# Optimization experiments

Hardware: AMD Instinct MI355X
Metric: run time of the kernel (lower is better)

Reference implementation:

```python
import jax, jax.numpy as jnp
import numpy as np

B, C, D = 2, 2048, 1024   # batch, seq_len, hidden_size
I = 2048                  # intermediate_size (GLU hidden)
E, K = 8, 2               # n_experts, top_k
CF = 1.25                 # capacity factor


def setup_inputs() -> dict:
    key = jax.random.key(0)
    k1, k2, k3, k4 = jax.random.split(key, 4)
    scale = 0.02
    return {
        "hidden_states": jax.random.normal(k1, (B, C, D), jnp.float32),
        "Wg": jax.random.normal(k2, (E, D), jnp.float32) * scale,      # router gate weight [E, d]
        "W1": jax.random.normal(k3, (E, D, 2 * I), jnp.float32) * scale,  # expert in-proj
        "W2": jax.random.normal(k4, (E, I, D), jnp.float32) * scale,      # expert out-proj
    }


def reference(hidden_states, Wg, W1, W2):
    Bx, Cx, d = hidden_states.shape
    N = Bx * Cx
    cap = int(N * K * CF / E)  # exp_capacity (static)
    x = hidden_states.reshape(N, d)

    # --- router (eval mode: no noise) ---
    logits = x @ Wg.T                          # [N, E]
    top_v, top_i = jax.lax.top_k(logits, K)    # [N, K]
    gates = jax.nn.softmax(top_v, axis=-1)     # [N, K]

    # --- greedy capacity-limited assignment (token-major, then k), vectorized ---
    flat_e = top_i.reshape(N * K)              # expert id per (token, k) slot, in loop order
    gates_f = gates.reshape(N * K)
    tok = jnp.repeat(jnp.arange(N), K)         # token id per slot
    onehot = jax.nn.one_hot(flat_e, E, dtype=jnp.int32)
    pos = jnp.cumsum(onehot, axis=0) - 1       # running count per expert
    pos_f = jnp.take_along_axis(pos, flat_e[:, None], axis=1)[:, 0]
    keep = pos_f < cap                         # slots beyond capacity are dropped
    pos_safe = jnp.where(keep, pos_f, cap)     # out-of-range -> dropped by mode='drop'

    # --- dispatch: exp_batches[e, pos] = x[token] ---
    exp_batches = jnp.zeros((E, cap, d), x.dtype).at[flat_e, pos_safe].set(x[tok], mode='drop')

    # --- per-expert GLU MLP (batched over experts) ---
    h = jnp.einsum('ecd,edf->ecf', exp_batches, W1)       # [E, cap, 2I]
    inp, gate = jnp.split(h, 2, axis=-1)
    h = jax.nn.gelu(inp, approximate=False) * gate        # exact gelu, matches torch
    exp_out = jnp.einsum('eci,eid->ecd', h, W2)           # [E, cap, d]

    # --- combine: equals exp_mask.view(N,-1) @ exp_out.view(-1,d) ---
    gathered = exp_out[flat_e, jnp.minimum(pos_safe, cap - 1)]  # [N*K, d]
    contrib = jnp.where(keep, gates_f, 0.0)[:, None] * gathered
    out = jax.ops.segment_sum(contrib, tok, num_segments=N)    # [N, d]
    return out.reshape(Bx, Cx, d)
```

## Files before the change

### kernel.cpp

```cpp
#include <hip/hip_runtime.h>
#include <hip/hip_bf16.h>
#include <math.h>

#define N_TOK 4096
#define DIM   1024
#define NEXP  8
#define IDIM  2048
#define TWOI  4096
#define CAP   1280

#define W1_BLOCKS (64 * 16 * NEXP)
#define W2_BLOCKS (16 * 32 * NEXP)

using short8  = __attribute__((ext_vector_type(8))) short;
using floatx4 = __attribute__((ext_vector_type(4))) float;

__device__ __forceinline__ unsigned short f2b(float f) {
  __hip_bfloat16 h = __float2bfloat16(f);
  return *reinterpret_cast<unsigned short*>(&h);
}

__device__ __forceinline__ void async16(const unsigned short* g, unsigned short* l) {
  __builtin_amdgcn_global_load_lds(
      (const __attribute__((address_space(1))) unsigned int*)g,
      (__attribute__((address_space(3))) unsigned int*)l,
      16, 0, 0);
}

__global__ __launch_bounds__(256) void trans_kernel(const float* __restrict__ W1,
                                                    const float* __restrict__ W2,
                                                    unsigned short* __restrict__ w1t,
                                                    unsigned short* __restrict__ w2t) {
  __shared__ float tile[64][65];
  int bid = blockIdx.x;
  const float* s; unsigned short* d; int R, C, r0, c0;
  if (bid < W1_BLOCKS) {
    int e = bid >> 10;
    int t = bid & 1023;
    R = DIM; C = TWOI;
    r0 = (t & 15) * 64;
    c0 = (t >> 4) * 64;
    s = W1 + (size_t)e * R * C;
    d = w1t + (size_t)e * R * C;
  } else {
    int b2 = bid - W1_BLOCKS;
    int e = b2 >> 9;
    int t = b2 & 511;
    R = IDIM; C = DIM;
    r0 = (t & 31) * 64;
    c0 = (t >> 5) * 64;
    s = W2 + (size_t)e * R * C;
    d = w2t + (size_t)e * R * C;
  }
  int tid = threadIdx.x;
  int tr = tid >> 4, tc = (tid & 15) * 4;
#pragma unroll
  for (int i = 0; i < 4; i++) {
    float4 v = *reinterpret_cast<const float4*>(&s[(size_t)(r0 + tr + i * 16) * C + c0 + tc]);
    tile[tr + i * 16][tc]     = v.x;
    tile[tr + i * 16][tc + 1] = v.y;
    tile[tr + i * 16][tc + 2] = v.z;
    tile[tr + i * 16][tc + 3] = v.w;
  }
  __syncthreads();
#pragma unroll
  for (int j = 0; j < 4; j++) {
    int c = (tid >> 4) + j * 16;
    int r4 = (tid & 15) * 4;
    ushort4 o;
    o.x = f2b(tile[r4][c]);
    o.y = f2b(tile[r4 + 1][c]);
    o.z = f2b(tile[r4 + 2][c]);
    o.w = f2b(tile[r4 + 3][c]);
    *reinterpret_cast<ushort4*>(&d[(size_t)(c0 + c) * R + r0 + r4]) = o;
  }
}

__global__ __launch_bounds__(256) void router_kernel(const float* __restrict__ x,
                                                     const float* __restrict__ Wg,
                                                     unsigned short* __restrict__ xb,
                                                     float* __restrict__ out,
                                                     int* __restrict__ top_i,
                                                     float* __restrict__ gates) {
  __shared__ float wg[NEXP * DIM];
  int tid = threadIdx.x;
  for (int i = tid * 4; i < NEXP * DIM; i += 256 * 4) {
    *reinterpret_cast<float4*>(wg + i) = *reinterpret_cast<const float4*>(Wg + i);
  }
  __syncthreads();
  int wave = tid >> 6, lane = tid & 63;
  int t = blockIdx.x * 4 + wave;
  const float* xr = x + (size_t)t * DIM;
  unsigned short* xbr = xb + (size_t)t * DIM;
  float* outr = out + (size_t)t * DIM;
  double acc[NEXP];
#pragma unroll
  for (int e = 0; e < NEXP; e++) acc[e] = 0.0;
  for (int i = lane; i < DIM; i += 64) {
    float xf = xr[i];
    xbr[i] = f2b(xf);
    outr[i] = 0.0f;
    double xv = (double)xf;
#pragma unroll
    for (int e = 0; e < NEXP; e++) acc[e] += xv * (double)wg[e * DIM + i];
  }
#pragma unroll
  for (int e = 0; e < NEXP; e++) {
#pragma unroll
    for (int m = 1; m < 64; m <<= 1) acc[e] += __shfl_xor(acc[e], m, 64);
  }
  if (lane == 0) {
    int i0 = 0; double v0 = acc[0];
    for (int e = 1; e < NEXP; e++) { if (acc[e] > v0) { v0 = acc[e]; i0 = e; } }
    int i1 = -1; double v1 = -1e300;
    for (int e = 0; e < NEXP; e++) { if (e != i0 && acc[e] > v1) { v1 = acc[e]; i1 = e; } }
    double e1 = exp(v1 - v0);
    float g0 = (float)(1.0 / (1.0 + e1));
    float g1 = (float)(e1 / (1.0 + e1));
    top_i[t * 2] = i0; top_i[t * 2 + 1] = i1;
    gates[t * 2] = g0; gates[t * 2 + 1] = g1;
  }
}

__global__ __launch_bounds__(1024) void scan_kernel(const int* __restrict__ top_i,
                                                    const float* __restrict__ gates,
                                                    int* __restrict__ rowtok,
                                                    float* __restrict__ rowgate,
                                                    int* __restrict__ cnt) {
  __shared__ int hist[NEXP][1024];
  int t = threadIdx.x;
  int s0 = t * 8;
  int eloc[8];
  int c[NEXP];
#pragma unroll
  for (int e = 0; e < NEXP; e++) c[e] = 0;
#pragma unroll
  for (int j = 0; j < 8; j++) { int e = top_i[s0 + j]; eloc[j] = e; c[e]++; }
#pragma unroll
  for (int e = 0; e < NEXP; e++) hist[e][t] = c[e];
  __syncthreads();
  for (int step = 1; step < 1024; step <<= 1) {
    int tmp[NEXP];
#pragma unroll
    for (int e = 0; e < NEXP; e++) tmp[e] = (t >= step) ? hist[e][t - step] : 0;
    __syncthreads();
#pragma unroll
    for (int e = 0; e < NEXP; e++) hist[e][t] += tmp[e];
    __syncthreads();
  }
  int base[NEXP];
#pragma unroll
  for (int e = 0; e < NEXP; e++) base[e] = hist[e][t] - c[e];
  if (t < NEXP) {
    int tot = hist[t][1023];
    cnt[t] = tot < CAP ? tot : CAP;
  }
#pragma unroll
  for (int j = 0; j < 8; j++) {
    int s = s0 + j;
    int e = eloc[j];
    int pos = base[e]++;
    if (pos < CAP) {
      rowtok[e * CAP + pos] = s >> 1;
      rowgate[e * CAP + pos] = gates[s];
    }
  }
}

__global__ __launch_bounds__(256, 3) void gemm1_kernel(const unsigned short* __restrict__ xb,
                                                       const unsigned short* __restrict__ w1t,
                                                       const int* __restrict__ rowtok,
                                                       const int* __restrict__ cnt,
                                                       unsigned short* __restrict__ H) {
  int e  = blockIdx.z;
  int m0 = blockIdx.y * 128;
  int i0 = blockIdx.x * 64;
  int cnte = cnt[e];
  if (m0 >= cnte) return;

  __shared__ __align__(16) unsigned short As[128 * 32];
  __shared__ __align__(16) unsigned short Bi[64 * 32];
  __shared__ __align__(16) unsigned short Bg[64 * 32];

  int tid  = threadIdx.x;
  int lane = tid & 63;
  int wave = tid >> 6;

  int srA0 = wave * 32 + (lane >> 2);
  int srA1 = srA0 + 16;
  int srB  = wave * 16 + (lane >> 2);
  int sk   = (lane & 3) * 8;

  int ma0 = m0 + srA0, ma1 = m0 + srA1;
  int tok0 = (ma0 < cnte) ? rowtok[e * CAP + ma0] : 0;
  int tok1 = (ma1 < cnte) ? rowtok[e * CAP + ma1] : 0;

  const unsigned short* w1e = w1t + (size_t)e * TWOI * DIM;
  const unsigned short* gA0 = xb + (size_t)tok0 * DIM + sk;
  const unsigned short* gA1 = xb + (size_t)tok1 * DIM + sk;
  const unsigned short* gBi = w1e + (size_t)(i0 + srB) * DIM + sk;
  const unsigned short* gBg = w1e + (size_t)(i0 + srB + IDIM) * DIM + sk;

  unsigned short* lA0 = As + (wave * 2 + 0) * 512;
  unsigned short* lA1 = As + (wave * 2 + 1) * 512;
  unsigned short* lBi = Bi + wave * 512;
  unsigned short* lBg = Bg + wave * 512;

  int lane16 = lane & 15;
  int quad   = lane >> 4;
  int wm = (wave & 1) * 64;
  int wn = (wave >> 1) * 32;

  floatx4 acc_i[4][2], acc_g[4][2];
#pragma unroll
  for (int i = 0; i < 4; i++)
#pragma unroll
    for (int j = 0; j < 2; j++) {
      acc_i[i][j] = (floatx4){0.f, 0.f, 0.f, 0.f};
      acc_g[i][j] = (floatx4){0.f, 0.f, 0.f, 0.f};
    }

  for (int k0 = 0; k0 < DIM; k0 += 32) {
    __syncthreads();
    async16(gA0 + k0, lA0);
    async16(gA1 + k0, lA1);
    async16(gBi + k0, lBi);
    async16(gBg + k0, lBg);
    __syncthreads();

    short8 a[4];
#pragma unroll
    for (int i = 0; i < 4; i++)
      a[i] = *(const short8*)&As[(wm + i * 16 + lane16) * 32 + quad * 8];
#pragma unroll
    for (int j = 0; j < 2; j++) {
      short8 bi = *(const short8*)&Bi[(wn + j * 16 + lane16) * 32 + quad * 8];
#pragma unroll
      for (int i = 0; i < 4; i++)
        acc_i[i][j] = __builtin_amdgcn_mfma_f32_16x16x32_bf16(a[i], bi, acc_i[i][j], 0, 0, 0);
      short8 bg = *(const short8*)&Bg[(wn + j * 16 + lane16) * 32 + quad * 8];
#pragma unroll
      for (int i = 0; i < 4; i++)
        acc_g[i][j] = __builtin_amdgcn_mfma_f32_16x16x32_bf16(a[i], bg, acc_g[i][j], 0, 0, 0);
    }
  }

  unsigned short* He = H + (size_t)e * CAP * IDIM;
#pragma unroll
  for (int i = 0; i < 4; i++) {
#pragma unroll
    for (int r = 0; r < 4; r++) {
      int m = m0 + wm + i * 16 + quad * 4 + r;
#pragma unroll
      for (int j = 0; j < 2; j++) {
        int n = i0 + wn + j * 16 + lane16;
        float vi = acc_i[i][j][r];
        float vg = acc_g[i][j][r];
        float h = 0.5f * vi * (1.0f + erff(vi * 0.70710678118654752f)) * vg;
        He[(size_t)m * IDIM + n] = f2b(h);
      }
    }
  }
}

__global__ __launch_bounds__(256, 3) void gemm2_kernel(const unsigned short* __restrict__ H,
                                                       const unsigned short* __restrict__ w2t,
                                                       const int* __restrict__ cnt,
                                                       const int* __restrict__ rowtok,
                                                       const float* __restrict__ rowgate,
                                                       float* __restrict__ out) {
  int e  = blockIdx.z;
  int m0 = blockIdx.y * 128;
  int n0 = blockIdx.x * 128;
  int cnte = cnt[e];
  if (m0 >= cnte) return;

  __shared__ __align__(16) unsigned short As[128 * 32];
  __shared__ __align__(16) unsigned short Bs[128 * 32];

  int tid  = threadIdx.x;
  int lane = tid & 63;
  int wave = tid >> 6;

  int sr0 = wave * 32 + (lane >> 2);
  int sr1 = sr0 + 16;
  int sk  = (lane & 3) * 8;

  const unsigned short* He  = H + (size_t)e * CAP * IDIM;
  const unsigned short* w2e = w2t + (size_t)e * DIM * IDIM;
  const unsigned short* gA0 = He + (size_t)(m0 + sr0) * IDIM + sk;
  const unsigned short* gA1 = He + (size_t)(m0 + sr1) * IDIM + sk;
  const unsigned short* gB0 = w2e + (size_t)(n0 + sr0) * IDIM + sk;
  const unsigned short* gB1 = w2e + (size_t)(n0 + sr1) * IDIM + sk;

  unsigned short* lA0 = As + (wave * 2 + 0) * 512;
  unsigned short* lA1 = As + (wave * 2 + 1) * 512;
  unsigned short* lB0 = Bs + (wave * 2 + 0) * 512;
  unsigned short* lB1 = Bs + (wave * 2 + 1) * 512;

  int lane16 = lane & 15;
  int quad   = lane >> 4;
  int wm = (wave & 1) * 64;
  int wn = (wave >> 1) * 64;

  floatx4 acc[4][4];
#pragma unroll
  for (int i = 0; i < 4; i++)
#pragma unroll
    for (int j = 0; j < 4; j++) acc[i][j] = (floatx4){0.f, 0.f, 0.f, 0.f};

  for (int k0 = 0; k0 < IDIM; k0 += 32) {
    __syncthreads();
    async16(gA0 + k0, lA0);
    async16(gA1 + k0, lA1);
    async16(gB0 + k0, lB0);
    async16(gB1 + k0, lB1);
    __syncthreads();

    short8 a[4];
#pragma unroll
    for (int i = 0; i < 4; i++)
      a[i] = *(const short8*)&As[(wm + i * 16 + lane16) * 32 + quad * 8];
#pragma unroll
    for (int j = 0; j < 4; j++) {
      short8 b = *(const short8*)&Bs[(wn + j * 16 + lane16) * 32 + quad * 8];
#pragma unroll
      for (int i = 0; i < 4; i++)
        acc[i][j] = __builtin_amdgcn_mfma_f32_16x16x32_bf16(a[i], b, acc[i][j], 0, 0, 0);
    }
  }

#pragma unroll
  for (int i = 0; i < 4; i++) {
#pragma unroll
    for (int r = 0; r < 4; r++) {
      int m = m0 + wm + i * 16 + quad * 4 + r;
      if (m < cnte) {
        int tok = rowtok[e * CAP + m];
        float g = rowgate[e * CAP + m];
        float* orow = out + (size_t)tok * DIM;
#pragma unroll
        for (int j = 0; j < 4; j++) {
          int n = n0 + wn + j * 16 + lane16;
          atomicAdd(orow + n, g * acc[i][j][r]);
        }
      }
    }
  }
}

extern "C" void kernel_launch(void* const* d_in, const int* in_sizes, int n_in,
                              void* d_out, int out_size, void* d_ws, size_t ws_size,
                              hipStream_t stream) {
  const float* x  = (const float*)d_in[0];
  const float* Wg = (const float*)d_in[1];
  const float* W1 = (const float*)d_in[2];
  const float* W2 = (const float*)d_in[3];
  float* out = (float*)d_out;

  char* ws = (char*)d_ws;
  size_t off = 0;
  auto alloc = [&](size_t bytes) -> void* {
    void* p = ws + off;
    off = (off + bytes + 255) & ~(size_t)255;
    return p;
  };
  int*   top_i   = (int*)alloc((size_t)N_TOK * 2 * sizeof(int));
  float* gates   = (float*)alloc((size_t)N_TOK * 2 * sizeof(float));
  int*   rowtok  = (int*)alloc((size_t)NEXP * CAP * sizeof(int));
  float* rowgate = (float*)alloc((size_t)NEXP * CAP * sizeof(float));
  int*   cnt     = (int*)alloc((size_t)NEXP * sizeof(int));
  unsigned short* xb  = (unsigned short*)alloc((size_t)N_TOK * DIM * 2);
  unsigned short* w1t = (unsigned short*)alloc((size_t)NEXP * TWOI * DIM * 2);
  unsigned short* w2t = (unsigned short*)alloc((size_t)NEXP * DIM * IDIM * 2);
  unsigned short* Hb  = (unsigned short*)alloc((size_t)NEXP * CAP * IDIM * 2);
  if (off > ws_size) return;

  hipLaunchKernelGGL(trans_kernel, dim3(W1_BLOCKS + W2_BLOCKS), dim3(256), 0, stream,
                     W1, W2, w1t, w2t);
  hipLaunchKernelGGL(router_kernel, dim3(N_TOK / 4), dim3(256), 0, stream,
                     x, Wg, xb, out, top_i, gates);
  hipLaunchKernelGGL(scan_kernel, dim3(1), dim3(1024), 0, stream,
                     top_i, gates, rowtok, rowgate, cnt);
  hipLaunchKernelGGL(gemm1_kernel, dim3(IDIM / 64, CAP / 128, NEXP), dim3(256), 0, stream,
                     xb, w1t, rowtok, cnt, Hb);
  hipLaunchKernelGGL(gemm2_kernel, dim3(DIM / 128, CAP / 128, NEXP), dim3(256), 0, stream,
                     Hb, w2t, cnt, rowtok, rowgate, out);
}
```

Baseline: 468.8 us.

## Fuse router into W1 transpose, overlap W2 transpose with gemm1, split-K gemm2

Merges the W1 transpose and the router into one prologue kernel, and moves the W2 transpose into extra z-slices of the gemm1 grid so it runs alongside the first expert GEMM. gemm2 is split in two along K (grid z doubles to 16), which raises the number of blocks. Each half covers only IDIM/2, so correctness depends on the unseen epilogue combining partial results, presumably by atomic adds into out. gemm1's occupancy hint goes from 3 to 4, and its shared memory is merged into one buffer sized for the transpose tile.

```diff
diff --git a/kernel.cpp b/kernel.cpp
--- a/kernel.cpp
+++ b/kernel.cpp
@@ -11,6 +11,11 @@
 
 #define W1_BLOCKS (64 * 16 * NEXP)
 #define W2_BLOCKS (16 * 32 * NEXP)
+#define ROUTER_BLOCKS (N_TOK / 4)
+
+#define G1X 32
+#define G1Y 10
+#define G1_TRANS_Z ((W2_BLOCKS + G1X * G1Y - 1) / (G1X * G1Y))
 
 using short8  = __attribute__((ext_vector_type(8))) short;
 using floatx4 = __attribute__((ext_vector_type(4))) float;
@@ -27,98 +32,87 @@
       16, 0, 0);
 }
 
-__global__ __launch_bounds__(256) void trans_kernel(const float* __restrict__ W1,
-                                                    const float* __restrict__ W2,
-                                                    unsigned short* __restrict__ w1t,
-                                                    unsigned short* __restrict__ w2t) {
-  __shared__ float tile[64][65];
+__global__ __launch_bounds__(256) void prologue_kernel(const float* __restrict__ W1,
+                                                       unsigned short* __restrict__ w1t,
+                                                       const float* __restrict__ x,
+                                                       const float* __restrict__ Wg,
+                                                       unsigned short* __restrict__ xb,
+                                                       float* __restrict__ out,
+                                                       int* __restrict__ top_i,
+                                                       float* __restrict__ gates) {
+  __shared__ __align__(16) float smem_f[NEXP * DIM];
   int bid = blockIdx.x;
-  const float* s; unsigned short* d; int R, C, r0, c0;
+  int tid = threadIdx.x;
+
   if (bid < W1_BLOCKS) {
+    float (*tile)[65] = reinterpret_cast<float (*)[65]>(smem_f);
     int e = bid >> 10;
     int t = bid & 1023;
-    R = DIM; C = TWOI;
-    r0 = (t & 15) * 64;
-    c0 = (t >> 4) * 64;
-    s = W1 + (size_t)e * R * C;
-    d = w1t + (size_t)e * R * C;
+    const int R = DIM, C = TWOI;
+    int r0 = (t & 15) * 64;
+    int c0 = (t >> 4) * 64;
+    const float* s = W1 + (size_t)e * R * C;
+    unsigned short* d = w1t + (size_t)e * R * C;
+    int tr = tid >> 4, tc = (tid & 15) * 4;
+#pragma unroll
+    for (int i = 0; i < 4; i++) {
+      float4 v = *reinterpret_cast<const float4*>(&s[(size_t)(r0 + tr + i * 16) * C + c0 + tc]);
+      tile[tr + i * 16][tc]     = v.x;
+      tile[tr + i * 16][tc + 1] = v.y;
+      tile[tr + i * 16][tc + 2] = v.z;
+      tile[tr + i * 16][tc + 3] = v.w;
+    }
+    __syncthreads();
+#pragma unroll
+    for (int j = 0; j < 4; j++) {
+      int c = (tid >> 4) + j * 16;
+      int r4 = (tid & 15) * 4;
+      ushort4 o;
+      o.x = f2b(tile[r4][c]);
+      o.y = f2b(tile[r4 + 1][c]);
+      o.z = f2b(tile[r4 + 2][c]);
+      o.w = f2b(tile[r4 + 3][c]);
+      *reinterpret_cast<ushort4*>(&d[(size_t)(c0 + c) * R + r0 + r4]) = o;
+    }
   } else {
-    int b2 = bid - W1_BLOCKS;
-    int e = b2 >> 9;
-    int t = b2 & 511;
-    R = IDIM; C = DIM;
-    r0 = (t & 31) * 64;
-    c0 = (t >> 5) * 64;
-    s = W2 + (size_t)e * R * C;
-    d = w2t + (size_t)e * R * C;
-  }
-  int tid = threadIdx.x;
-  int tr = tid >> 4, tc = (tid & 15) * 4;
-#pragma unroll
-  for (int i = 0; i < 4; i++) {
-    float4 v = *reinterpret_cast<const float4*>(&s[(size_t)(r0 + tr + i * 16) * C + c0 + tc]);
-    tile[tr + i * 16][tc]     = v.x;
-    tile[tr + i * 16][tc + 1] = v.y;
-    tile[tr + i * 16][tc + 2] = v.z;
-    tile[tr + i * 16][tc + 3] = v.w;
-  }
-  __syncthreads();
-#pragma unroll
-  for (int j = 0; j < 4; j++) {
-    int c = (tid >> 4) + j * 16;
-    int r4 = (tid & 15) * 4;
-    ushort4 o;
-    o.x = f2b(tile[r4][c]);
-    o.y = f2b(tile[r4 + 1][c]);
-    o.z = f2b(tile[r4 + 2][c]);
-    o.w = f2b(tile[r4 + 3][c]);
-    *reinterpret_cast<ushort4*>(&d[(size_t)(c0 + c) * R + r0 + r4]) = o;
-  }
-}
-
-__global__ __launch_bounds__(256) void router_kernel(const float* __restrict__ x,
-                                                     const float* __restrict__ Wg,
-                                                     unsigned short* __restrict__ xb,
-                                                     float* __restrict__ out,
-                                                     int* __restrict__ top_i,
-                                                     float* __restrict__ gates) {
-  __shared__ float wg[NEXP * DIM];
-  int tid = threadIdx.x;
-  for (int i = tid * 4; i < NEXP * DIM; i += 256 * 4) {
-    *reinterpret_cast<float4*>(wg + i) = *reinterpret_cast<const float4*>(Wg + i);
-  }
-  __syncthreads();
-  int wave = tid >> 6, lane = tid & 63;
-  int t = blockIdx.x * 4 + wave;
-  const float* xr = x + (size_t)t * DIM;
-  unsigned short* xbr = xb + (size_t)t * DIM;
-  float* outr = out + (size_t)t * DIM;
-  double acc[NEXP];
-#pragma unroll
-  for (int e = 0; e < NEXP; e++) acc[e] = 0.0;
-  for (int i = lane; i < DIM; i += 64) {
-    float xf = xr[i];
-    xbr[i] = f2b(xf);
-    outr[i] = 0.0f;
-    double xv = (double)xf;
-#pragma unroll
-    for (int e = 0; e < NEXP; e++) acc[e] += xv * (double)wg[e * DIM + i];
-  }
-#pragma unroll
-  for (int e = 0; e < NEXP; e++) {
-#pragma unroll
-    for (int m = 1; m < 64; m <<= 1) acc[e] += __shfl_xor(acc[e], m, 64);
-  }
-  if (lane == 0) {
-    int i0 = 0; double v0 = acc[0];
-    for (int e = 1; e < NEXP; e++) { if (acc[e] > v0) { v0 = acc[e]; i0 = e; } }
-    int i1 = -1; double v1 = -1e300;
-    for (int e = 0; e < NEXP; e++) { if (e != i0 && acc[e] > v1) { v1 = acc[e]; i1 = e; } }
-    double e1 = exp(v1 - v0);
-    float g0 = (float)(1.0 / (1.0 + e1));
-    float g1 = (float)(e1 / (1.0 + e1));
-    top_i[t * 2] = i0; top_i[t * 2 + 1] = i1;
-    gates[t * 2] = g0; gates[t * 2 + 1] = g1;
+    int rb = bid - W1_BLOCKS;
+    float* wg = smem_f;
+    for (int i = tid * 4; i < NEXP * DIM; i += 256 * 4) {
+      *reinterpret_cast<float4*>(wg + i) = *reinterpret_cast<const float4*>(Wg + i);
+    }
+    __syncthreads();
+    int wave = tid >> 6, lane = tid & 63;
+    int t = rb * 4 + wave;
+    const float* xr = x + (size_t)t * DIM;
+    unsigned short* xbr = xb + (size_t)t * DIM;
+    float* outr = out + (size_t)t * DIM;
+    double acc[NEXP];
+#pragma unroll
+    for (int e = 0; e < NEXP; e++) acc[e] = 0.0;
+    for (int i = lane; i < DIM; i += 64) {
+      float xf = xr[i];
+      xbr[i] = f2b(xf);
+      outr[i] = 0.0f;
+      double xv = (double)xf;
+#pragma unroll
+      for (int e = 0; e < NEXP; e++) acc[e] += xv * (double)wg[e * DIM + i];
+    }
+#pragma unroll
+    for (int e = 0; e < NEXP; e++) {
+#pragma unroll
+      for (int m = 1; m < 64; m <<= 1) acc[e] += __shfl_xor(acc[e], m, 64);
+    }
+    if (lane == 0) {
+      int i0 = 0; double v0 = acc[0];
+      for (int e = 1; e < NEXP; e++) { if (acc[e] > v0) { v0 = acc[e]; i0 = e; } }
+      int i1 = -1; double v1 = -1e300;
+      for (int e = 0; e < NEXP; e++) { if (e != i0 && acc[e] > v1) { v1 = acc[e]; i1 = e; } }
+      double e1 = exp(v1 - v0);
+      float g0 = (float)(1.0 / (1.0 + e1));
+      float g1 = (float)(e1 / (1.0 + e1));
+      top_i[t * 2] = i0; top_i[t * 2 + 1] = i1;
+      gates[t * 2] = g0; gates[t * 2 + 1] = g1;
+    }
   }
 }
 
@@ -167,22 +161,62 @@
   }
 }
 
-__global__ __launch_bounds__(256, 3) void gemm1_kernel(const unsigned short* __restrict__ xb,
+__global__ __launch_bounds__(256, 4) void gemm1_kernel(const unsigned short* __restrict__ xb,
                                                        const unsigned short* __restrict__ w1t,
                                                        const int* __restrict__ rowtok,
                                                        const int* __restrict__ cnt,
-                                                       unsigned short* __restrict__ H) {
-  int e  = blockIdx.z;
+                                                       unsigned short* __restrict__ H,
+                                                       const float* __restrict__ W2,
+                                                       unsigned short* __restrict__ w2t) {
+  __shared__ __align__(16) unsigned char smem[64 * 65 * 4];
+  int tid  = threadIdx.x;
+  int z = blockIdx.z;
+
+  if (z >= NEXP) {
+    int id = (z - NEXP) * (G1X * G1Y) + blockIdx.y * G1X + blockIdx.x;
+    if (id >= W2_BLOCKS) return;
+    float (*tile)[65] = reinterpret_cast<float (*)[65]>(smem);
+    int e = id >> 9;
+    int t = id & 511;
+    const int R = IDIM, C = DIM;
+    int r0 = (t & 31) * 64;
+    int c0 = (t >> 5) * 64;
+    const float* s = W2 + (size_t)e * R * C;
+    unsigned short* d = w2t + (size_t)e * R * C;
+    int tr = tid >> 4, tc = (tid & 15) * 4;
+#pragma unroll
+    for (int i = 0; i < 4; i++) {
+      float4 v = *reinterpret_cast<const float4*>(&s[(size_t)(r0 + tr + i * 16) * C + c0 + tc]);
+      tile[tr + i * 16][tc]     = v.x;
+      tile[tr + i * 16][tc + 1] = v.y;
+      tile[tr + i * 16][tc + 2] = v.z;
+      tile[tr + i * 16][tc + 3] = v.w;
+    }
+    __syncthreads();
+#pragma unroll
+    for (int j = 0; j < 4; j++) {
+      int c = (tid >> 4) + j * 16;
+      int r4 = (tid & 15) * 4;
+      ushort4 o;
+      o.x = f2b(tile[r4][c]);
+      o.y = f2b(tile[r4 + 1][c]);
+      o.z = f2b(tile[r4 + 2][c]);
+      o.w = f2b(tile[r4 + 3][c]);
+      *reinterpret_cast<ushort4*>(&d[(size_t)(c0 + c) * R + r0 + r4]) = o;
+    }
+    return;
+  }
+
+  int e  = z;
   int m0 = blockIdx.y * 128;
   int i0 = blockIdx.x * 64;
   int cnte = cnt[e];
   if (m0 >= cnte) return;
 
-  __shared__ __align__(16) unsigned short As[128 * 32];
-  __shared__ __align__(16) unsigned short Bi[64 * 32];
-  __shared__ __align__(16) unsigned short Bg[64 * 32];
-
-  int tid  = threadIdx.x;
+  unsigned short* As = reinterpret_cast<unsigned short*>(smem);
+  unsigned short* Bi = reinterpret_cast<unsigned short*>(smem + 8192);
+  unsigned short* Bg = reinterpret_cast<unsigned short*>(smem + 12288);
+
   int lane = tid & 63;
   int wave = tid >> 6;
 
@@ -269,7 +303,8 @@
                                                        const int* __restrict__ rowtok,
                                                        const float* __restrict__ rowgate,
                                                        float* __restrict__ out) {
-  int e  = blockIdx.z;
+  int e  = blockIdx.z & 7;
+  int kh = blockIdx.z >> 3;
   int m0 = blockIdx.y * 128;
   int n0 = blockIdx.x * 128;
   int cnte = cnt[e];
@@ -285,13 +320,14 @@
   int sr0 = wave * 32 + (lane >> 2);
   int sr1 = sr0 + 16;
   int sk  = (lane & 3) * 8;
+  int kbase = kh * (IDIM / 2);
 
   const unsigned short* He  = H + (size_t)e * CAP * IDIM;
   const unsigned short* w2e = w2t + (size_t)e * DIM * IDIM;
-  const unsigned short* gA0 = He + (size_t)(m0 + sr0) * IDIM + sk;
-  const unsigned short* gA1 = He + (size_t)(m0 + sr1) * IDIM + sk;
-  const unsigned short* gB0 = w2e + (size_t)(n0 + sr0) * IDIM + sk;
-  const unsigned short* gB1 = w2e + (size_t)(n0 + sr1) * IDIM + sk;
+  const unsigned short* gA0 = He + (size_t)(m0 + sr0) * IDIM + kbase + sk;
+  const unsigned short* gA1 = He + (size_t)(m0 + sr1) * IDIM + kbase + sk;
+  const unsigned short* gB0 = w2e + (size_t)(n0 + sr0) * IDIM + kbase + sk;
+  const unsigned short* gB1 = w2e + (size_t)(n0 + sr1) * IDIM + kbase + sk;
 
   unsigned short* lA0 = As + (wave * 2 + 0) * 512;
   unsigned short* lA1 = As + (wave * 2 + 1) * 512;
@@ -309,7 +345,7 @@
 #pragma unroll
     for (int j = 0; j < 4; j++) acc[i][j] = (floatx4){0.f, 0.f, 0.f, 0.f};
 
-  for (int k0 = 0; k0 < IDIM; k0 += 32) {
+  for (int k0 = 0; k0 < IDIM / 2; k0 += 32) {
     __syncthreads();
     async16(gA0 + k0, lA0);
     async16(gA1 + k0, lA1);
@@ -376,14 +412,12 @@
   unsigned short* Hb  = (unsigned short*)alloc((size_t)NEXP * CAP * IDIM * 2);
   if (off > ws_size) return;
 
-  hipLaunchKernelGGL(trans_kernel, dim3(W1_BLOCKS + W2_BLOCKS), dim3(256), 0, stream,
-                     W1, W2, w1t, w2t);
-  hipLaunchKernelGGL(router_kernel, dim3(N_TOK / 4), dim3(256), 0, stream,
-                     x, Wg, xb, out, top_i, gates);
+  hipLaunchKernelGGL(prologue_kernel, dim3(W1_BLOCKS + ROUTER_BLOCKS), dim3(256), 0, stream,
+                     W1, w1t, x, Wg, xb, out, top_i, gates);
   hipLaunchKernelGGL(scan_kernel, dim3(1), dim3(1024), 0, stream,
                      top_i, gates, rowtok, rowgate, cnt);
-  hipLaunchKernelGGL(gemm1_kernel, dim3(IDIM / 64, CAP / 128, NEXP), dim3(256), 0, stream,
-                     xb, w1t, rowtok, cnt, Hb);
-  hipLaunchKernelGGL(gemm2_kernel, dim3(DIM / 128, CAP / 128, NEXP), dim3(256), 0, stream,
+  hipLaunchKernelGGL(gemm1_kernel, dim3(G1X, G1Y, NEXP + G1_TRANS_Z), dim3(256), 0, stream,
+                     xb, w1t, rowtok, cnt, Hb, W2, w2t);
+  hipLaunchKernelGGL(gemm2_kernel, dim3(DIM / 128, CAP / 128, 16), dim3(256), 0, stream,
                      Hb, w2t, cnt, rowtok, rowgate, out);
 }
```

Measured after the change: 471.5 us. No clear change (+0.6%).
